# Kernel tuning notes

Hardware: AMD Instinct MI355X
Metric: run time of the kernel (lower is better)

The kernel has to match this reference:

```python
import jax, jax.numpy as jnp
import numpy as np
from jax import lax

V, E, H, T = 50000, 256, 512, 16  # vocab, embed_dim, hidden_dim, num_tags
B, S = 32, 512
C = 128          # conv channels
HD = H // 2      # per-direction LSTM hidden


def setup_inputs() -> dict:
    key = jax.random.key(0)
    ks = jax.random.split(key, 20)
    g = lambda k, shape, s=0.05: jax.random.normal(k, shape, jnp.float32) * s
    return {
        "x": jax.random.randint(ks[0], (B, S), 0, V),
        "mask": jnp.ones((B, S), jnp.int32),
        "tags": jax.random.randint(ks[1], (B, S), 0, T),
        "embed_table": g(ks[2], (V, E), 0.1),
        "conv_w": g(ks[3], (C, E, 3)),
        "conv_b": g(ks[4], (C,)),
        "wih_f": g(ks[5], (4 * HD, C)),
        "whh_f": g(ks[6], (4 * HD, HD)),
        "bih_f": g(ks[7], (4 * HD,)),
        "bhh_f": g(ks[8], (4 * HD,)),
        "wih_b": g(ks[9], (4 * HD, C)),
        "whh_b": g(ks[10], (4 * HD, HD)),
        "bih_b": g(ks[11], (4 * HD,)),
        "bhh_b": g(ks[12], (4 * HD,)),
        "fc_w": g(ks[13], (T, H)),
        "fc_b": g(ks[14], (T,)),
        "start_trans": g(ks[15], (T,), 0.1),
        "end_trans": g(ks[16], (T,), 0.1),
        "trans": g(ks[17], (T, T), 0.1),
    }


def _lstm_dir(xs, wih, whh, bih, bhh, reverse):
    # xs: [S, B, D] -> hidden states [S, B, HD], PyTorch gate order i,f,g,o
    b = xs.shape[1]
    h0 = jnp.zeros((b, whh.shape[1]), xs.dtype)

    def step(carry, xt):
        h, c = carry
        gates = xt @ wih.T + h @ whh.T + bih + bhh  # [B, 4*HD]
        i, f, g, o = jnp.split(gates, 4, axis=-1)
        c = jax.nn.sigmoid(f) * c + jax.nn.sigmoid(i) * jnp.tanh(g)
        h = jax.nn.sigmoid(o) * jnp.tanh(c)
        return (h, c), h

    _, hs = lax.scan(step, (h0, h0), xs, reverse=reverse)
    return hs


def _crf_nll(emissions, tg, m, start_trans, end_trans, trans):
    # emissions [S,B,T], tg [S,B] int, m [S,B] float -> per-seq -loglik mean
    bidx = jnp.arange(emissions.shape[1])
    # numerator: score of the gold path
    score = start_trans[tg[0]] + emissions[0, bidx, tg[0]]

    def num_step(s, inp):
        prev_t, cur_t, em, mi = inp
        return s + (trans[prev_t, cur_t] + em[bidx, cur_t]) * mi, None

    score, _ = lax.scan(num_step, score, (tg[:-1], tg[1:], emissions[1:], m[1:]))
    seq_ends = m.sum(0).astype(jnp.int32) - 1
    score = score + end_trans[tg[seq_ends, bidx]]
    # denominator: forward algorithm (log partition)
    alpha = start_trans + emissions[0]  # [B,T]

    def den_step(a, inp):
        em, mi = inp
        nxt = jax.nn.logsumexp(a[:, :, None] + trans[None] + em[:, None, :], axis=1)
        return jnp.where(mi[:, None] > 0, nxt, a), None

    alpha, _ = lax.scan(den_step, alpha, (emissions[1:], m[1:]))
    logz = jax.nn.logsumexp(alpha + end_trans[None], axis=1)
    return -jnp.mean(score - logz)


def reference(x, mask, tags, embed_table, conv_w, conv_b, wih_f, whh_f, bih_f,
              bhh_f, wih_b, whh_b, bih_b, bhh_b, fc_w, fc_b, start_trans,
              end_trans, trans):
    emb = embed_table[x]                       # [B,S,E]
    xc = jnp.transpose(emb, (0, 2, 1))         # [B,E,S]
    conv = lax.conv_general_dilated(xc, conv_w, (1,), [(1, 1)],
                                    dimension_numbers=("NCH", "OIH", "NCH"))
    feat = jax.nn.relu(conv + conv_b[None, :, None])   # [B,C,S]
    xs = jnp.transpose(feat, (2, 0, 1))        # [S,B,C]
    hf = _lstm_dir(xs, wih_f, whh_f, bih_f, bhh_f, False)
    hb = _lstm_dir(xs, wih_b, whh_b, bih_b, bhh_b, True)
    h = jnp.concatenate([hf, hb], axis=-1)     # [S,B,H]
    emissions = h @ fc_w.T + fc_b              # [S,B,T]
    m = jnp.transpose(mask, (1, 0)).astype(emissions.dtype)
    tg = jnp.transpose(tags, (1, 0))
    return _crf_nll(emissions, tg, m, start_trans, end_trans, trans)
```

## Files before the change

### kernel.cpp

```cpp
#include <hip/hip_runtime.h>
#include <hip/hip_bf16.h>

constexpr int NB = 32, NS = 512, NE = 256, NC = 128, NHD = 256, NG = 1024, NT = 16, NH = 512;

typedef float f32x4 __attribute__((ext_vector_type(4)));

__device__ __forceinline__ unsigned short f2bf(float f) {
    unsigned u = __float_as_uint(f);
    u += 0x7fffu + ((u >> 16) & 1u);
    return (unsigned short)(u >> 16);
}
__device__ __forceinline__ float bf2f(unsigned short s) {
    return __uint_as_float(((unsigned)s) << 16);
}
__device__ __forceinline__ float vexp2(float x) {
    float r; asm("v_exp_f32 %0, %1" : "=v"(r) : "v"(x)); return r;
}
__device__ __forceinline__ float vrcp(float x) {
    float r; asm("v_rcp_f32 %0, %1" : "=v"(r) : "v"(x)); return r;
}
__device__ __forceinline__ float vlog2(float x) {
    float r; asm("v_log_f32 %0, %1" : "=v"(r) : "v"(x)); return r;
}
__device__ __forceinline__ unsigned char f2fp8(float v) {
    int r = __builtin_amdgcn_cvt_pk_fp8_f32(v, 0.f, 0, false);
    return (unsigned char)(r & 0xff);
}
__device__ __constant__ float KSC[4] = {-1.442695041f, -1.442695041f, 2.885390082f, -1.442695041f};

__global__ void k_prep_convw(const float* __restrict__ w, float* __restrict__ wT) {
    int i = blockIdx.x * 256 + threadIdx.x;
    if (i >= 768 * 128) return;
    int e3 = i >> 7, c = i & 127;
    wT[i] = w[c * 768 + e3];
}

__global__ void k_prep_scale(const float* __restrict__ whh_f, const float* __restrict__ whh_b,
                             float* __restrict__ scale) {
    int d = blockIdx.y;
    const float* src = d ? whh_b : whh_f;
    int col = blockIdx.x * 256 + threadIdx.x;
    if (col >= 1024) return;
    int j = col >> 2, g = col & 3;
    const float* p = src + (size_t)(g * 256 + j) * 256;
    float m = 0.f;
    for (int k = 0; k < 256; ++k) m = fmaxf(m, fabsf(p[k]));
    scale[d * 1024 + col] = (m > 0.f) ? (m * (1.f / 448.f)) : 1.f;
}

__global__ void k_prep_whh_frag8(const float* __restrict__ whh_f, const float* __restrict__ whh_b,
                                 const float* __restrict__ scale, unsigned char* __restrict__ whhF8) {
    int i = blockIdx.x * 256 + threadIdx.x;
    if (i >= (1 << 19)) return;
    int e = i & 7;
    int lane = (i >> 3) & 63;
    int g = (i >> 9) & 3;
    int kt = (i >> 11) & 7;
    int cg = (i >> 14) & 1;
    int w = (i >> 15) & 7;
    int d = (i >> 18) & 1;
    const float* src = d ? whh_b : whh_f;
    int j = w * 32 + cg * 16 + (lane & 15);
    int k = kt * 32 + (lane >> 4) * 8 + e;
    float sc = scale[d * 1024 + j * 4 + g];
    float v = src[(g * 256 + j) * 256 + k] / sc;
    whhF8[i] = f2fp8(v);
}

__global__ void k_prep_wih(const float* __restrict__ wih_f, const float* __restrict__ wih_b,
                           float* __restrict__ wihT) {
    int d = blockIdx.y;
    const float* src = d ? wih_b : wih_f;
    int i = blockIdx.x * 256 + threadIdx.x;
    if (i >= NC * NG) return;
    int g = i & 3, j = (i >> 2) & 255, e = i >> 10;
    wihT[(size_t)d * NC * NG + i] = src[(g * 256 + j) * 128 + e];
}

__global__ void k_prep_bias(const float* __restrict__ bih_f, const float* __restrict__ bhh_f,
                            const float* __restrict__ bih_b, const float* __restrict__ bhh_b,
                            float* __restrict__ bias2) {
    int d = blockIdx.y;
    const float* bi = d ? bih_b : bih_f;
    const float* bh = d ? bhh_b : bhh_f;
    int i = blockIdx.x * 256 + threadIdx.x;
    if (i >= NG) return;
    int g = i & 3, j = i >> 2;
    bias2[(size_t)d * NG + i] = bi[g * 256 + j] + bh[g * 256 + j];
}

__global__ __launch_bounds__(128) void k_conv(const int* __restrict__ x,
                                              const float* __restrict__ table,
                                              const float* __restrict__ wT,
                                              const float* __restrict__ conv_b,
                                              float* __restrict__ feat) {
    int b = blockIdx.y;
    int s0 = blockIdx.x * 8;
    int c = threadIdx.x;
    __shared__ float win[10][NE];
    for (int i = 0; i < 10; ++i) {
        int s = s0 - 1 + i;
        if (s < 0 || s >= NS) {
            for (int e = c; e < NE; e += 128) win[i][e] = 0.f;
        } else {
            int tok = x[b * NS + s];
            const float* row = table + (size_t)tok * NE;
            for (int e = c; e < NE; e += 128) win[i][e] = row[e];
        }
    }
    __syncthreads();
    float acc[8];
    float bc = conv_b[c];
#pragma unroll
    for (int p = 0; p < 8; ++p) acc[p] = bc;
    for (int e = 0; e < NE; ++e) {
        float r[10];
#pragma unroll
        for (int i = 0; i < 10; ++i) r[i] = win[i][e];
#pragma unroll
        for (int k = 0; k < 3; ++k) {
            float wv = wT[(e * 3 + k) * NC + c];
#pragma unroll
            for (int p = 0; p < 8; ++p) acc[p] += wv * r[p + k];
        }
    }
#pragma unroll
    for (int p = 0; p < 8; ++p) {
        feat[((size_t)b * NS + s0 + p) * NC + c] = fmaxf(acc[p], 0.f);
    }
}

__global__ __launch_bounds__(256) void k_xgate(const float* __restrict__ feat,
                                               const float* __restrict__ wihT,
                                               const float* __restrict__ bias2,
                                               unsigned short* __restrict__ xg) {
    int d = blockIdx.y;
    int p0 = blockIdx.x * 16;
    int j = threadIdx.x;
    __shared__ float fv[16][NC];
    for (int i = threadIdx.x; i < 16 * NC; i += 256) {
        int p = i >> 7, e = i & 127;
        int idx = p0 + p;
        int s = idx >> 5, b = idx & 31;
        fv[p][e] = feat[((size_t)b * NS + s) * NC + e];
    }
    __syncthreads();
    const float* W = wihT + (size_t)d * NC * NG;
    float b0 = bias2[(size_t)d * NG + j * 4 + 0];
    float b1 = bias2[(size_t)d * NG + j * 4 + 1];
    float b2 = bias2[(size_t)d * NG + j * 4 + 2];
    float b3 = bias2[(size_t)d * NG + j * 4 + 3];
    float acc[16][4];
#pragma unroll
    for (int p = 0; p < 16; ++p) {
        acc[p][0] = b0; acc[p][1] = b1; acc[p][2] = b2; acc[p][3] = b3;
    }
    for (int e = 0; e < NC; ++e) {
        float4 w4 = *(const float4*)(W + ((size_t)e * 256 + j) * 4);
#pragma unroll
        for (int p = 0; p < 16; ++p) {
            float fe = fv[p][e];
            acc[p][0] += fe * w4.x;
            acc[p][1] += fe * w4.y;
            acc[p][2] += fe * w4.z;
            acc[p][3] += fe * w4.w;
        }
    }
#pragma unroll
    for (int p = 0; p < 16; ++p) {
        ushort4 o;
        o.x = f2bf(acc[p][0] * KSC[0]); o.y = f2bf(acc[p][1] * KSC[1]);
        o.z = f2bf(acc[p][2] * KSC[2]); o.w = f2bf(acc[p][3] * KSC[3]);
        unsigned short* dst = xg + (size_t)d * NS * NB * NG + ((size_t)(p0 + p) * 256 + j) * 4;
        *(ushort4*)dst = o;
    }
}

__global__ __launch_bounds__(512, 1) void k_lstm2(const unsigned char* __restrict__ whhF8,
                                                  const float* __restrict__ scale,
                                                  const unsigned short* __restrict__ xg,
                                                  float* __restrict__ hcat) {
    int bid = blockIdx.x;
    int d = bid >> 1, bh = bid & 1;
    int tid = threadIdx.x;
    int w = tid >> 6, l = tid & 63;
    int l15 = l & 15, lq = l >> 4;
    __shared__ unsigned char hbuf[2][16][272];
    for (int i = tid; i < 2 * 16 * 272; i += 512) (&hbuf[0][0][0])[i] = 0;
    unsigned long long wf[64];
    const unsigned char* wp = whhF8 + ((size_t)(d * 8 + w) << 15) + (size_t)l * 8;
#pragma unroll
    for (int f = 0; f < 64; ++f) wf[f] = *(const unsigned long long*)(wp + f * 512);
    float csc[2][4];
#pragma unroll
    for (int cg = 0; cg < 2; ++cg)
#pragma unroll
        for (int g = 0; g < 4; ++g)
            csc[cg][g] = scale[d * 1024 + (w * 32 + cg * 16 + l15) * 4 + g] * KSC[g];
    const unsigned short* XG = xg + (size_t)d * NS * NB * NG;
    float cst[2][4] = {};
    __syncthreads();
    int cur = 0;
    unsigned long long xq[2][4];
    {
        int s0 = d ? (NS - 1) : 0;
#pragma unroll
        for (int cg = 0; cg < 2; ++cg)
#pragma unroll
            for (int r = 0; r < 4; ++r)
                xq[cg][r] = *(const unsigned long long*)(
                    XG + (size_t)(s0 * 32 + bh * 16 + lq * 4 + r) * 1024 + (w * 32 + cg * 16 + l15) * 4);
    }
    for (int step = 0; step < NS; ++step) {
        int s = d ? (NS - 1 - step) : step;
        unsigned long long xn[2][4];
        {
            int stn = (step + 1 < NS) ? step + 1 : step;
            int sn = d ? (NS - 1 - stn) : stn;
#pragma unroll
            for (int cg = 0; cg < 2; ++cg)
#pragma unroll
                for (int r = 0; r < 4; ++r)
                    xn[cg][r] = *(const unsigned long long*)(
                        XG + (size_t)(sn * 32 + bh * 16 + lq * 4 + r) * 1024 + (w * 32 + cg * 16 + l15) * 4);
        }
        f32x4 acc[2][4];
#pragma unroll
        for (int cg = 0; cg < 2; ++cg)
#pragma unroll
            for (int g = 0; g < 4; ++g)
                acc[cg][g] = (f32x4){0.f, 0.f, 0.f, 0.f};
#pragma unroll
        for (int kt = 0; kt < 8; ++kt) {
            unsigned long long a = *(const unsigned long long*)&hbuf[cur][l15][kt * 32 + lq * 8];
#pragma unroll
            for (int cg = 0; cg < 2; ++cg)
#pragma unroll
                for (int g = 0; g < 4; ++g)
                    acc[cg][g] = __builtin_amdgcn_mfma_f32_16x16x32_fp8_fp8(
                        (long long)a, (long long)wf[cg * 32 + kt * 4 + g], acc[cg][g], 0, 0, 0);
        }
        int nxt = cur ^ 1;
#pragma unroll
        for (int cg = 0; cg < 2; ++cg) {
            int cell = w * 32 + cg * 16 + l15;
#pragma unroll
            for (int r = 0; r < 4; ++r) {
                unsigned long long xv = xq[cg][r];
                float pi = fmaf(acc[cg][0][r], csc[cg][0], bf2f((unsigned short)xv));
                float pf = fmaf(acc[cg][1][r], csc[cg][1], bf2f((unsigned short)(xv >> 16)));
                float pg = fmaf(acc[cg][2][r], csc[cg][2], bf2f((unsigned short)(xv >> 32)));
                float po = fmaf(acc[cg][3][r], csc[cg][3], bf2f((unsigned short)(xv >> 48)));
                float si = vrcp(1.f + vexp2(pi));
                float sf = vrcp(1.f + vexp2(pf));
                float tg = fmaf(-2.f, vrcp(1.f + vexp2(pg)), 1.f);
                float so = vrcp(1.f + vexp2(po));
                float c = fmaf(sf, cst[cg][r], si * tg);
                cst[cg][r] = c;
                float tc = fmaf(-2.f, vrcp(1.f + vexp2(2.885390082f * c)), 1.f);
                float h = so * tc;
                int b = lq * 4 + r;
                __builtin_nontemporal_store(h,
                    hcat + (size_t)(s * 32 + bh * 16 + b) * NH + d * NHD + cell);
                hbuf[nxt][b][cell] = f2fp8(h);
            }
        }
        __syncthreads();
        cur = nxt;
#pragma unroll
        for (int cg = 0; cg < 2; ++cg)
#pragma unroll
            for (int r = 0; r < 4; ++r) xq[cg][r] = xn[cg][r];
    }
}

__global__ __launch_bounds__(256) void k_fc(const float* __restrict__ hcat,
                                            const float* __restrict__ fc_w,
                                            const float* __restrict__ fc_b,
                                            float* __restrict__ em) {
    int p0 = blockIdx.x * 16;
    __shared__ float hv[16][NH];
    for (int i = threadIdx.x; i < 16 * NH; i += 256) {
        int p = i >> 9, hh = i & 511;
        hv[p][hh] = hcat[(size_t)(p0 + p) * NH + hh];
    }
    __syncthreads();
    int p = threadIdx.x >> 4, t = threadIdx.x & 15;
    const float* fw = fc_w + t * NH;
    float acc = fc_b[t];
#pragma unroll 8
    for (int hh = 0; hh < NH; ++hh) acc += hv[p][hh] * fw[hh];
    em[(size_t)(p0 + p) * NT + t] = acc;
}

__global__ __launch_bounds__(64) void k_crf(const float* __restrict__ em,
                                            const int* __restrict__ tags,
                                            const int* __restrict__ mask,
                                            const float* __restrict__ start_t,
                                            const float* __restrict__ end_t,
                                            const float* __restrict__ trans,
                                            float* __restrict__ res) {
    int b = blockIdx.x;
    int tid = threadIdx.x;
    __shared__ float em_sh[NS * NT];
    __shared__ float tr[NT * NT];
    __shared__ float alpha_sh[NT];
    __shared__ float msk[NS];
    __shared__ float sc_sh;
    for (int i = tid; i < NT * NT; i += 64) tr[i] = trans[i];
    for (int i = tid; i < NS * NT; i += 64) {
        int s = i >> 4, t = i & 15;
        em_sh[i] = em[((size_t)s * NB + b) * NT + t];
    }
    for (int s = tid; s < NS; s += 64) msk[s] = (float)mask[b * NS + s];
    __syncthreads();
    float part = 0.f, msum = 0.f;
    for (int s = tid; s < NS; s += 64) msum += msk[s];
    for (int s = 1 + tid; s < NS; s += 64) {
        int pv = tags[b * NS + s - 1], cu = tags[b * NS + s];
        part += (tr[pv * NT + cu] + em_sh[s * NT + cu]) * msk[s];
    }
#pragma unroll
    for (int o = 32; o > 0; o >>= 1) {
        part += __shfl_down(part, o);
        msum += __shfl_down(msum, o);
    }
    if (tid == 0) {
        int t0 = tags[b * NS];
        int send = (int)msum - 1;
        sc_sh = start_t[t0] + em_sh[t0] + part + end_t[tags[b * NS + send]];
    }
    if (tid < NT) alpha_sh[tid] = start_t[tid] + em_sh[tid];
    __syncthreads();
    int t_to = tid >> 2, q = tid & 3;
    for (int s = 1; s < NS; ++s) {
        float v0 = alpha_sh[q * 4 + 0] + tr[(q * 4 + 0) * NT + t_to];
        float v1 = alpha_sh[q * 4 + 1] + tr[(q * 4 + 1) * NT + t_to];
        float v2 = alpha_sh[q * 4 + 2] + tr[(q * 4 + 2) * NT + t_to];
        float v3 = alpha_sh[q * 4 + 3] + tr[(q * 4 + 3) * NT + t_to];
        float mx = fmaxf(fmaxf(v0, v1), fmaxf(v2, v3));
        mx = fmaxf(mx, __shfl_xor(mx, 1));
        mx = fmaxf(mx, __shfl_xor(mx, 2));
        float nmx = -1.442695041f * mx;
        float ss = vexp2(fmaf(v0, 1.442695041f, nmx)) + vexp2(fmaf(v1, 1.442695041f, nmx))
                 + vexp2(fmaf(v2, 1.442695041f, nmx)) + vexp2(fmaf(v3, 1.442695041f, nmx));
        ss += __shfl_xor(ss, 1);
        ss += __shfl_xor(ss, 2);
        float nv = mx + 0.6931471806f * vlog2(ss) + em_sh[s * NT + t_to];
        float old = alpha_sh[t_to];
        nv = (msk[s] > 0.f) ? nv : old;
        __syncthreads();
        if (q == 0) alpha_sh[t_to] = nv;
        __syncthreads();
    }
    if (tid == 0) {
        float mx = -1e30f;
        for (int t = 0; t < NT; ++t) mx = fmaxf(mx, alpha_sh[t] + end_t[t]);
        float sum = 0.f;
        for (int t = 0; t < NT; ++t) sum += vexp2(1.442695041f * (alpha_sh[t] + end_t[t] - mx));
        res[b] = sc_sh - (mx + 0.6931471806f * vlog2(sum));
    }
}

__global__ void k_final(const float* __restrict__ res, float* __restrict__ out) {
    int tid = threadIdx.x;
    float v = (tid < NB) ? res[tid] : 0.f;
#pragma unroll
    for (int o = 32; o > 0; o >>= 1) v += __shfl_down(v, o);
    if (tid == 0) out[0] = -v / NB;
}

constexpr size_t SZ_FEAT  = (size_t)NB * NS * NC * 4;
constexpr size_t SZ_WT    = (size_t)768 * 128 * 4;
constexpr size_t SZ_WHHF8 = (size_t)(1 << 19);
constexpr size_t SZ_SCALE = (size_t)2 * 1024 * 4;
constexpr size_t SZ_WIHT  = (size_t)2 * NC * NG * 4;
constexpr size_t SZ_BIAS  = (size_t)2 * NG * 4;
constexpr size_t SZ_XG    = (size_t)2 * NS * NB * NG * 2;
constexpr size_t SZ_HCAT  = (size_t)NS * NB * NH * 4;
constexpr size_t SZ_EM    = (size_t)NS * NB * NT * 4;

constexpr size_t OFF_FEAT  = 0;
constexpr size_t OFF_WT    = OFF_FEAT + SZ_FEAT;
constexpr size_t OFF_WHHF8 = OFF_WT + SZ_WT;
constexpr size_t OFF_SCALE = OFF_WHHF8 + SZ_WHHF8;
constexpr size_t OFF_WIHT  = OFF_SCALE + SZ_SCALE;
constexpr size_t OFF_BIAS  = OFF_WIHT + SZ_WIHT;
constexpr size_t OFF_XG    = OFF_BIAS + SZ_BIAS;
constexpr size_t OFF_HCAT  = OFF_XG + SZ_XG;
constexpr size_t OFF_EM    = OFF_HCAT + SZ_HCAT;
constexpr size_t OFF_RES   = OFF_EM + SZ_EM;

extern "C" void kernel_launch(void* const* d_in, const int* in_sizes, int n_in,
                              void* d_out, int out_size, void* d_ws, size_t ws_size,
                              hipStream_t stream) {
    const int* x        = (const int*)d_in[0];
    const int* mask     = (const int*)d_in[1];
    const int* tags     = (const int*)d_in[2];
    const float* table  = (const float*)d_in[3];
    const float* conv_w = (const float*)d_in[4];
    const float* conv_b = (const float*)d_in[5];
    const float* wih_f  = (const float*)d_in[6];
    const float* whh_f  = (const float*)d_in[7];
    const float* bih_f  = (const float*)d_in[8];
    const float* bhh_f  = (const float*)d_in[9];
    const float* wih_b  = (const float*)d_in[10];
    const float* whh_b  = (const float*)d_in[11];
    const float* bih_b  = (const float*)d_in[12];
    const float* bhh_b  = (const float*)d_in[13];
    const float* fc_w   = (const float*)d_in[14];
    const float* fc_b   = (const float*)d_in[15];
    const float* start_t = (const float*)d_in[16];
    const float* end_t  = (const float*)d_in[17];
    const float* trans  = (const float*)d_in[18];

    char* ws = (char*)d_ws;
    float* feat = (float*)(ws + OFF_FEAT);
    float* wT   = (float*)(ws + OFF_WT);
    unsigned char* whhF8 = (unsigned char*)(ws + OFF_WHHF8);
    float* scale = (float*)(ws + OFF_SCALE);
    float* wihT = (float*)(ws + OFF_WIHT);
    float* bias2 = (float*)(ws + OFF_BIAS);
    unsigned short* xg = (unsigned short*)(ws + OFF_XG);
    float* hcat = (float*)(ws + OFF_HCAT);
    float* em   = (float*)(ws + OFF_EM);
    float* res  = (float*)(ws + OFF_RES);

    k_prep_convw<<<dim3(384), 256, 0, stream>>>(conv_w, wT);
    k_prep_scale<<<dim3(4, 2), 256, 0, stream>>>(whh_f, whh_b, scale);
    k_prep_whh_frag8<<<dim3(2048), 256, 0, stream>>>(whh_f, whh_b, scale, whhF8);
    k_prep_wih<<<dim3(512, 2), 256, 0, stream>>>(wih_f, wih_b, wihT);
    k_prep_bias<<<dim3(4, 2), 256, 0, stream>>>(bih_f, bhh_f, bih_b, bhh_b, bias2);
    k_conv<<<dim3(NS / 8, NB), 128, 0, stream>>>(x, table, wT, conv_b, feat);
    k_xgate<<<dim3(NS * NB / 16, 2), 256, 0, stream>>>(feat, wihT, bias2, xg);
    k_lstm2<<<dim3(4), 512, 0, stream>>>(whhF8, scale, xg, hcat);
    k_fc<<<dim3(NS * NB / 16), 256, 0, stream>>>(hcat, fc_w, fc_b, em);
    k_crf<<<dim3(NB), 64, 0, stream>>>(em, tags, mask, start_t, end_t, trans, res);
    k_final<<<dim3(1), 64, 0, stream>>>(res, (float*)d_out);
}
```

Baseline: 1.552 ms.

## Split LSTM recurrence across 16 waves with one 16-cell group each

Result: faster. 1.381 ms (-11.0%).

```diff
diff --git a/kernel.cpp b/kernel.cpp
--- a/kernel.cpp
+++ b/kernel.cpp
@@ -56,11 +56,10 @@
     int lane = (i >> 3) & 63;
     int g = (i >> 9) & 3;
     int kt = (i >> 11) & 7;
-    int cg = (i >> 14) & 1;
-    int w = (i >> 15) & 7;
+    int w = (i >> 14) & 15;
     int d = (i >> 18) & 1;
     const float* src = d ? whh_b : whh_f;
-    int j = w * 32 + cg * 16 + (lane & 15);
+    int j = w * 16 + (lane & 15);
     int k = kt * 32 + (lane >> 4) * 8 + e;
     float sc = scale[d * 1024 + j * 4 + g];
     float v = src[(g * 256 + j) * 256 + k] / sc;
@@ -176,101 +175,85 @@
     }
 }
 
-__global__ __launch_bounds__(512, 1) void k_lstm2(const unsigned char* __restrict__ whhF8,
-                                                  const float* __restrict__ scale,
-                                                  const unsigned short* __restrict__ xg,
-                                                  float* __restrict__ hcat) {
+__global__ __launch_bounds__(1024, 1) void k_lstm2(const unsigned char* __restrict__ whhF8,
+                                                   const float* __restrict__ scale,
+                                                   const unsigned short* __restrict__ xg,
+                                                   float* __restrict__ hcat) {
     int bid = blockIdx.x;
     int d = bid >> 1, bh = bid & 1;
     int tid = threadIdx.x;
     int w = tid >> 6, l = tid & 63;
     int l15 = l & 15, lq = l >> 4;
-    __shared__ unsigned char hbuf[2][16][272];
-    for (int i = tid; i < 2 * 16 * 272; i += 512) (&hbuf[0][0][0])[i] = 0;
-    unsigned long long wf[64];
-    const unsigned char* wp = whhF8 + ((size_t)(d * 8 + w) << 15) + (size_t)l * 8;
-#pragma unroll
-    for (int f = 0; f < 64; ++f) wf[f] = *(const unsigned long long*)(wp + f * 512);
-    float csc[2][4];
-#pragma unroll
-    for (int cg = 0; cg < 2; ++cg)
-#pragma unroll
-        for (int g = 0; g < 4; ++g)
-            csc[cg][g] = scale[d * 1024 + (w * 32 + cg * 16 + l15) * 4 + g] * KSC[g];
+    __shared__ unsigned char hbuf[2][16][280];
+    for (int i = tid; i < 2 * 16 * 280; i += 1024) (&hbuf[0][0][0])[i] = 0;
+    unsigned long long wf[32];
+    const unsigned char* wp = whhF8 + ((size_t)(d * 16 + w) << 14) + (size_t)l * 8;
+#pragma unroll
+    for (int f = 0; f < 32; ++f) wf[f] = *(const unsigned long long*)(wp + f * 512);
+    int cell = w * 16 + l15;
+    float csc[4];
+#pragma unroll
+    for (int g = 0; g < 4; ++g)
+        csc[g] = scale[d * 1024 + cell * 4 + g] * KSC[g];
     const unsigned short* XG = xg + (size_t)d * NS * NB * NG;
-    float cst[2][4] = {};
+    float cst[4] = {};
     __syncthreads();
     int cur = 0;
-    unsigned long long xq[2][4];
+    unsigned long long xq[4];
     {
         int s0 = d ? (NS - 1) : 0;
 #pragma unroll
-        for (int cg = 0; cg < 2; ++cg)
-#pragma unroll
-            for (int r = 0; r < 4; ++r)
-                xq[cg][r] = *(const unsigned long long*)(
-                    XG + (size_t)(s0 * 32 + bh * 16 + lq * 4 + r) * 1024 + (w * 32 + cg * 16 + l15) * 4);
+        for (int r = 0; r < 4; ++r)
+            xq[r] = *(const unsigned long long*)(
+                XG + (size_t)(s0 * 32 + bh * 16 + lq * 4 + r) * 1024 + cell * 4);
     }
     for (int step = 0; step < NS; ++step) {
         int s = d ? (NS - 1 - step) : step;
-        unsigned long long xn[2][4];
+        unsigned long long xn[4];
         {
             int stn = (step + 1 < NS) ? step + 1 : step;
             int sn = d ? (NS - 1 - stn) : stn;
 #pragma unroll
-            for (int cg = 0; cg < 2; ++cg)
-#pragma unroll
-                for (int r = 0; r < 4; ++r)
-                    xn[cg][r] = *(const unsigned long long*)(
-                        XG + (size_t)(sn * 32 + bh * 16 + lq * 4 + r) * 1024 + (w * 32 + cg * 16 + l15) * 4);
-        }
-        f32x4 acc[2][4];
-#pragma unroll
-        for (int cg = 0; cg < 2; ++cg)
-#pragma unroll
-            for (int g = 0; g < 4; ++g)
-                acc[cg][g] = (f32x4){0.f, 0.f, 0.f, 0.f};
+            for (int r = 0; r < 4; ++r)
+                xn[r] = *(const unsigned long long*)(
+                    XG + (size_t)(sn * 32 + bh * 16 + lq * 4 + r) * 1024 + cell * 4);
+        }
+        f32x4 acc[4];
+#pragma unroll
+        for (int g = 0; g < 4; ++g) acc[g] = (f32x4){0.f, 0.f, 0.f, 0.f};
 #pragma unroll
         for (int kt = 0; kt < 8; ++kt) {
             unsigned long long a = *(const unsigned long long*)&hbuf[cur][l15][kt * 32 + lq * 8];
 #pragma unroll
-            for (int cg = 0; cg < 2; ++cg)
-#pragma unroll
-                for (int g = 0; g < 4; ++g)
-                    acc[cg][g] = __builtin_amdgcn_mfma_f32_16x16x32_fp8_fp8(
-                        (long long)a, (long long)wf[cg * 32 + kt * 4 + g], acc[cg][g], 0, 0, 0);
+            for (int g = 0; g < 4; ++g)
+                acc[g] = __builtin_amdgcn_mfma_f32_16x16x32_fp8_fp8(
+                    (long long)a, (long long)wf[kt * 4 + g], acc[g], 0, 0, 0);
         }
         int nxt = cur ^ 1;
 #pragma unroll
-        for (int cg = 0; cg < 2; ++cg) {
-            int cell = w * 32 + cg * 16 + l15;
-#pragma unroll
-            for (int r = 0; r < 4; ++r) {
-                unsigned long long xv = xq[cg][r];
-                float pi = fmaf(acc[cg][0][r], csc[cg][0], bf2f((unsigned short)xv));
-                float pf = fmaf(acc[cg][1][r], csc[cg][1], bf2f((unsigned short)(xv >> 16)));
-                float pg = fmaf(acc[cg][2][r], csc[cg][2], bf2f((unsigned short)(xv >> 32)));
-                float po = fmaf(acc[cg][3][r], csc[cg][3], bf2f((unsigned short)(xv >> 48)));
-                float si = vrcp(1.f + vexp2(pi));
-                float sf = vrcp(1.f + vexp2(pf));
-                float tg = fmaf(-2.f, vrcp(1.f + vexp2(pg)), 1.f);
-                float so = vrcp(1.f + vexp2(po));
-                float c = fmaf(sf, cst[cg][r], si * tg);
-                cst[cg][r] = c;
-                float tc = fmaf(-2.f, vrcp(1.f + vexp2(2.885390082f * c)), 1.f);
-                float h = so * tc;
-                int b = lq * 4 + r;
-                __builtin_nontemporal_store(h,
-                    hcat + (size_t)(s * 32 + bh * 16 + b) * NH + d * NHD + cell);
-                hbuf[nxt][b][cell] = f2fp8(h);
-            }
+        for (int r = 0; r < 4; ++r) {
+            unsigned long long xv = xq[r];
+            float pi = fmaf(acc[0][r], csc[0], bf2f((unsigned short)xv));
+            float pf = fmaf(acc[1][r], csc[1], bf2f((unsigned short)(xv >> 16)));
+            float pg = fmaf(acc[2][r], csc[2], bf2f((unsigned short)(xv >> 32)));
+            float po = fmaf(acc[3][r], csc[3], bf2f((unsigned short)(xv >> 48)));
+            float si = vrcp(1.f + vexp2(pi));
+            float sf = vrcp(1.f + vexp2(pf));
+            float tg = fmaf(-2.f, vrcp(1.f + vexp2(pg)), 1.f);
+            float so = vrcp(1.f + vexp2(po));
+            float c = fmaf(sf, cst[r], si * tg);
+            cst[r] = c;
+            float tc = fmaf(-2.f, vrcp(1.f + vexp2(2.885390082f * c)), 1.f);
+            float h = so * tc;
+            int b = lq * 4 + r;
+            __builtin_nontemporal_store(h,
+                hcat + (size_t)(s * 32 + bh * 16 + b) * NH + d * NHD + cell);
+            hbuf[nxt][b][cell] = f2fp8(h);
         }
         __syncthreads();
         cur = nxt;
 #pragma unroll
-        for (int cg = 0; cg < 2; ++cg)
-#pragma unroll
-            for (int r = 0; r < 4; ++r) xq[cg][r] = xn[cg][r];
+        for (int r = 0; r < 4; ++r) xq[r] = xn[r];
     }
 }
 
@@ -433,7 +416,7 @@
     k_prep_bias<<<dim3(4, 2), 256, 0, stream>>>(bih_f, bhh_f, bih_b, bhh_b, bias2);
     k_conv<<<dim3(NS / 8, NB), 128, 0, stream>>>(x, table, wT, conv_b, feat);
     k_xgate<<<dim3(NS * NB / 16, 2), 256, 0, stream>>>(feat, wihT, bias2, xg);
-    k_lstm2<<<dim3(4), 512, 0, stream>>>(whhF8, scale, xg, hcat);
+    k_lstm2<<<dim3(4), 1024, 0, stream>>>(whhF8, scale, xg, hcat);
     k_fc<<<dim3(NS * NB / 16), 256, 0, stream>>>(hcat, fc_w, fc_b, em);
     k_crf<<<dim3(NB), 64, 0, stream>>>(em, tags, mask, start_t, end_t, trans, res);
     k_final<<<dim3(1), 64, 0, stream>>>(res, (float*)d_out);
```
